# Performance work log

Measured on AMD Instinct MI355X. Metric: run time of the kernel, lower is better.

The kernel has to match this reference:

```python
import jax, jax.numpy as jnp
import numpy as np

R = 50000          # residues
P = 24             # residue_pad_length
APR = 15           # atoms per residue (<= P)
N = R * APR        # total atoms
ACD = ATD = RCD = RID = 32
N_ATOM_CODES, N_ATOM_TYPES, N_RES_CODES, MAX_SEQ = 38, 6, 21, 1024
VEC_OUT, SC_OUT = 64, 256          # irreps_out = 64x1e + 256x0e
SC_IN = P * ACD + P * ATD + RCD + RID  # 1600 scalar inputs


def setup_inputs() -> dict:
    key = jax.random.key(0)
    ks = jax.random.split(key, 10)
    return {
        "residue_base_coords": jax.random.normal(ks[0], (R, 3), jnp.float32),
        "residue_relative_coords": jax.random.normal(ks[1], (N, 3), jnp.float32),
        "residue_code_index": jax.random.randint(ks[2], (R,), 0, N_RES_CODES),
        "residue_sequence_index": jnp.arange(R) % MAX_SEQ,
        "atom_code_index": jax.random.randint(ks[3], (N,), 0, N_ATOM_CODES),
        "atom_type_index": jax.random.randint(ks[4], (N,), 0, N_ATOM_TYPES),
        "residue_index_atomwise": jnp.repeat(jnp.arange(R), APR),  # sorted, APR atoms each
        "W_atom_code": jax.random.normal(ks[5], (N_ATOM_CODES, ACD), jnp.float32),
        "W_atom_type": jax.random.normal(ks[6], (N_ATOM_TYPES, ATD), jnp.float32),
        "W_res_code": jax.random.normal(ks[7], (N_RES_CODES, RCD), jnp.float32),
        "W_res_idx": jax.random.normal(ks[8], (MAX_SEQ, RID), jnp.float32),
        "W_vec": jax.random.normal(jax.random.fold_in(key, 1), (P, VEC_OUT), jnp.float32),
        "W_sc": jax.random.normal(ks[9], (SC_IN, SC_OUT), jnp.float32),
    }


def reference(residue_base_coords, residue_relative_coords, residue_code_index,
              residue_sequence_index, atom_code_index, atom_type_index,
              residue_index_atomwise, W_atom_code, W_atom_type, W_res_code,
              W_res_idx, W_vec, W_sc):
    R_ = residue_base_coords.shape[0]
    P_ = W_vec.shape[0]
    N_ = residue_index_atomwise.shape[0]
    ri = residue_index_atomwise
    # vectorized replacement of the per-residue python loop:
    # position of each atom within its residue (residue_index_atomwise is sorted)
    offsets = jnp.searchsorted(ri, jnp.arange(R_))            # first atom of each residue
    pos = jnp.arange(N_) - offsets[ri]                        # [N]
    # scatter atoms into padded [R, P, ...] layout (pad slots stay 0, like F.pad)
    mask = jnp.zeros((R_, P_), bool).at[ri, pos].set(True)
    rel = jnp.zeros((R_, P_, 3), residue_relative_coords.dtype).at[ri, pos].set(residue_relative_coords)
    codes = jnp.zeros((R_, P_), atom_code_index.dtype).at[ri, pos].set(atom_code_index)
    types = jnp.zeros((R_, P_), atom_type_index.dtype).at[ri, pos].set(atom_type_index)
    maskf = mask.astype(W_atom_code.dtype)[..., None]
    # embedding lookups, masked (pad embeddings zeroed as in the torch code)
    ac = (W_atom_code[codes] * maskf).reshape(R_, -1)         # [R, P*ACD]
    at = (W_atom_type[types] * maskf).reshape(R_, -1)         # [R, P*ATD]
    rc = W_res_code[residue_code_index]                       # [R, RCD]
    rix = W_res_idx[residue_sequence_index]                   # [R, RID]
    scalars = jnp.concatenate([ac, at, rc, rix], axis=-1)     # [R, SC_IN]
    # e3nn o3.Linear: l=1 channels mix only with l=1 (Px1e -> VEC_OUTx1e),
    # l=0 channels mix only with l=0; path-normalized by sqrt(fan_in), no bias.
    out_vec = jnp.einsum('rpc,pm->rmc', rel, W_vec) / jnp.sqrt(jnp.float32(P_))
    out_sc = (scalars @ W_sc) / jnp.sqrt(jnp.float32(scalars.shape[-1]))
    features = jnp.concatenate([out_vec.reshape(R_, -1), out_sc], axis=-1)  # [R, 3*VEC_OUT+SC_OUT]
    return residue_base_coords, features  # ResidueState(coords, features)
```

## Files before the change

kernel.cpp:

```cpp
#include <hip/hip_runtime.h>
#include <stdint.h>

static constexpr int P       = 24;
static constexpr int EMB_D   = 32;
static constexpr int N_AC    = 38;
static constexpr int N_AT    = 6;
static constexpr int N_RC    = 21;
static constexpr int MAXSEQ  = 1024;
static constexpr int VEC_OUT = 64;
static constexpr int SC_OUT  = 256;
static constexpr int FEAT    = 3 * VEC_OUT + SC_OUT;
static constexpr int CT      = N_AC * N_AT;
static constexpr int NROWS   = P * CT;
static constexpr int ROWB    = SC_OUT * 2;
static constexpr uint32_t ZROWB = (uint32_t)NROWS * ROWB;
static constexpr uint32_t EOFS  = (uint32_t)N_RC * 512;

#define AS1 __attribute__((address_space(1)))
#define AS3 __attribute__((address_space(3)))

__device__ __forceinline__ unsigned short f2bf(float f) {
    uint32_t x = __float_as_uint(f);
    uint32_t r = (x + 0x7FFFu + ((x >> 16) & 1u)) >> 16;
    return (unsigned short)r;
}

__device__ __forceinline__ void gl_lds16(const void* g, void* l) {
    __builtin_amdgcn_global_load_lds((const AS1 void*)g, (AS3 void*)l, 16, 0, 0);
}

__global__ __launch_bounds__(256) void k1_init_build(
        const float* __restrict__ Wac, const float* __restrict__ Wat,
        const float* __restrict__ Wrc, const float* __restrict__ Wri,
        const float* __restrict__ Wsc,
        float* __restrict__ Ec, float* __restrict__ Et,
        unsigned short* __restrict__ ErcH, unsigned short* __restrict__ ErixH,
        int* __restrict__ starts, int* __restrict__ ends, int R) {
    int b = blockIdx.x;
    const int initB = (R + 255) / 256;
    if (b < initB) {
        int i = b * 256 + threadIdx.x;
        if (i < R) { starts[i] = 0; ends[i] = 0; }
        return;
    }
    b -= initB;
    const float* Wemb; int n_emb, sc_base, idx, sect;
    if (b < P * N_AC) {
        Wemb = Wac; n_emb = N_AC; sc_base = 0; idx = b; sect = 0;
    } else if (b < P * N_AC + P * N_AT) {
        Wemb = Wat; n_emb = N_AT; sc_base = P * EMB_D; idx = b - P * N_AC; sect = 1;
    } else if (b < P * N_AC + P * N_AT + N_RC) {
        Wemb = Wrc; n_emb = N_RC; sc_base = 2 * P * EMB_D;
        idx = b - (P * N_AC + P * N_AT); sect = 2;
    } else {
        Wemb = Wri; n_emb = MAXSEQ; sc_base = 2 * P * EMB_D + EMB_D;
        idx = b - (P * N_AC + P * N_AT + N_RC); sect = 3;
    }
    int p = idx / n_emb, e = idx % n_emb;
    int o = threadIdx.x;
    const float* wrow = Wemb + (size_t)e * EMB_D;
    const float* scol = Wsc + (size_t)(sc_base + p * EMB_D) * SC_OUT + o;
    float s = 0.f;
#pragma unroll
    for (int d = 0; d < EMB_D; ++d) s += wrow[d] * scol[(size_t)d * SC_OUT];
    s *= 0.025f;
    if (sect == 0)      Ec[(size_t)idx * SC_OUT + o] = s;
    else if (sect == 1) Et[(size_t)idx * SC_OUT + o] = s;
    else if (sect == 2) ErcH[(size_t)idx * SC_OUT + o] = f2bf(s);
    else                ErixH[(size_t)idx * SC_OUT + o] = f2bf(s);
}

__global__ void k2_find_bounds(const int* __restrict__ ri, int* __restrict__ starts,
                               int* __restrict__ ends, int N) {
    int i = blockIdx.x * blockDim.x + threadIdx.x;
    if (i >= N) return;
    int r = ri[i];
    if (i == 0 || ri[i - 1] != r) starts[r] = i;
    if (i == N - 1 || ri[i + 1] != r) ends[r] = i + 1;
}

__global__ __launch_bounds__(256) void k3_fuse_prep(
        const float* __restrict__ Ec, const float* __restrict__ Et,
        unsigned short* __restrict__ Etab,
        const int* __restrict__ starts, const int* __restrict__ ends,
        const int* __restrict__ rcode, const int* __restrict__ rseq,
        const int* __restrict__ acode, const int* __restrict__ atype,
        const float* __restrict__ rel, const float* __restrict__ base,
        float* __restrict__ out_coords,
        int4* __restrict__ hdr, uint32_t* __restrict__ recArr, int R) {
    int b = blockIdx.x;
    if (b < NROWS + 1) {
        int o = threadIdx.x;
        if (b == NROWS) { Etab[(size_t)b * SC_OUT + o] = 0; return; }
        int j = b / CT, ct = b % CT, c = ct / N_AT, t = ct % N_AT;
        float s = Ec[((size_t)j * N_AC + c) * SC_OUT + o] +
                  Et[((size_t)j * N_AT + t) * SC_OUT + o];
        Etab[(size_t)b * SC_OUT + o] = f2bf(s);
        return;
    }
    b -= NROWS + 1;
    const int hdrB = (R + 255) >> 8;
    if (b < hdrB) {
        int i = b * 256 + threadIdx.x;
        if (i < R) {
            int st = starts[i];
            int c = ends[i] - st; if (c > P) c = P;
            hdr[i] = make_int4(st, c, rcode[i], rseq[i]);
        }
        return;
    }
    b -= hdrB;
    const int coordB = (3 * R + 1023) >> 10;
    if (b < coordB) {
        int i = b * 256 + threadIdx.x;
        int n4 = (3 * R) >> 2;
        if (i < n4)
            reinterpret_cast<float4*>(out_coords)[i] =
                reinterpret_cast<const float4*>(base)[i];
        if (i == n4) {
            for (int t = 4 * n4; t < 3 * R; ++t) out_coords[t] = base[t];
        }
        return;
    }
    b -= coordB;
    int i = b * 256 + threadIdx.x;
    if (i >= R * 64) return;
    int r = i >> 6, l = i & 63;
    int st = starts[r];
    int c = ends[r] - st; if (c > P) c = P;
    uint32_t out;
    if (l < 16) {
        out = ZROWB;
        if (l < c)
            out = (uint32_t)((l * CT + acode[st + l] * N_AT + atype[st + l]) * ROWB);
    } else {
        int idx = l - 16, k = idx / 3, cc = idx - k * 3;
        float v = 0.f;
        if (k < c) v = rel[(size_t)(st + k) * 3 + cc];
        out = __float_as_uint(v);
    }
    recArr[(size_t)r * 64 + l] = out;
}

struct F3 { float x, y, z; };

__global__ __launch_bounds__(256, 4) void k4_residue(
        const int4* __restrict__ hdr, const uint32_t* __restrict__ recArr,
        const unsigned char* __restrict__ tab,
        const unsigned char* __restrict__ ErcBase,
        const float* __restrict__ Wvec,
        const int* __restrict__ acode, const int* __restrict__ atype,
        const float* __restrict__ rel,
        float* __restrict__ out_feat, int R) {

    __shared__ uint8_t stage[4][9 * 1024];
    const int wid    = threadIdx.x >> 6;
    const int lane   = threadIdx.x & 63;
    const int b31    = lane & 31;
    const bool hiH   = lane >= 32;
    const uint32_t lo16 = (uint32_t)(b31 * 16);
    const int wave   = (blockIdx.x << 2) + wid;
    const int totalw = gridDim.x << 2;
    if (wave >= R) return;
    uint8_t* buf = stage[wid];

    float w[16];
#pragma unroll
    for (int k = 0; k < 16; ++k) w[k] = Wvec[k * VEC_OUT + lane];

    int j = wave;
    int r0 = __builtin_amdgcn_readfirstlane(j < R ? j : R - 1);
    uint32_t rec = recArr[(size_t)r0 * 64 + lane];
    int4 h = hdr[r0];

    while (true) {
        int jn = j + totalw;
        int r1 = __builtin_amdgcn_readfirstlane(jn < R ? jn : R - 1);
        uint32_t recN = recArr[(size_t)r1 * 64 + lane];
        int4 hN = hdr[r1];

#pragma unroll
        for (int k = 0; k < 8; ++k) {
            uint32_t re = (uint32_t)__builtin_amdgcn_readlane((int)rec, 2 * k);
            uint32_t ro = (uint32_t)__builtin_amdgcn_readlane((int)rec, 2 * k + 1);
            gl_lds16(tab + (hiH ? ro : re) + lo16, buf + k * 1024);
        }
        {
            uint32_t vo = (hiH ? EOFS + ((uint32_t)h.w << 9)
                               : ((uint32_t)h.z << 9)) + lo16;
            gl_lds16(ErcBase + vo, buf + 8 * 1024);
        }

        float vx = 0.f, vy = 0.f, vz = 0.f;
#pragma unroll
        for (int k = 0; k < 16; ++k) {
            float sx = __uint_as_float((uint32_t)__builtin_amdgcn_readlane((int)rec, 16 + 3 * k));
            float sy = __uint_as_float((uint32_t)__builtin_amdgcn_readlane((int)rec, 17 + 3 * k));
            float sz = __uint_as_float((uint32_t)__builtin_amdgcn_readlane((int)rec, 18 + 3 * k));
            vx = fmaf(sx, w[k], vx);
            vy = fmaf(sy, w[k], vy);
            vz = fmaf(sz, w[k], vz);
        }

        asm volatile("s_waitcnt vmcnt(0)" ::: "memory");
        __builtin_amdgcn_sched_barrier(0);

        float a0 = 0.f, a1 = 0.f, a2 = 0.f, a3 = 0.f;
        float a4 = 0.f, a5 = 0.f, a6 = 0.f, a7 = 0.f;
#pragma unroll
        for (int k = 0; k < 9; ++k) {
            uint4 gk = *reinterpret_cast<const uint4*>(buf + k * 1024 + lane * 16);
            a0 += __uint_as_float(gk.x << 16);
            a1 += __uint_as_float(gk.x & 0xFFFF0000u);
            a2 += __uint_as_float(gk.y << 16);
            a3 += __uint_as_float(gk.y & 0xFFFF0000u);
            a4 += __uint_as_float(gk.z << 16);
            a5 += __uint_as_float(gk.z & 0xFFFF0000u);
            a6 += __uint_as_float(gk.w << 16);
            a7 += __uint_as_float(gk.w & 0xFFFF0000u);
        }

        a0 += __shfl_xor(a0, 32); a1 += __shfl_xor(a1, 32);
        a2 += __shfl_xor(a2, 32); a3 += __shfl_xor(a3, 32);
        a4 += __shfl_xor(a4, 32); a5 += __shfl_xor(a5, 32);
        a6 += __shfl_xor(a6, 32); a7 += __shfl_xor(a7, 32);

        if (h.y > 16) {
            int st = h.x;
            for (int k = 16; k < h.y; ++k) {
                int c = acode[st + k], t = atype[st + k];
                const unsigned char* rp = tab +
                    (uint32_t)((k * CT + c * N_AT + t) * ROWB) + lo16;
                uint4 gg = *reinterpret_cast<const uint4*>(rp);
                float wk = Wvec[k * VEC_OUT + lane];
                vx = fmaf(rel[(size_t)(st + k) * 3], wk, vx);
                vy = fmaf(rel[(size_t)(st + k) * 3 + 1], wk, vy);
                vz = fmaf(rel[(size_t)(st + k) * 3 + 2], wk, vz);
                float t0 = __uint_as_float(gg.x << 16);
                float t1 = __uint_as_float(gg.x & 0xFFFF0000u);
                float t2 = __uint_as_float(gg.y << 16);
                float t3 = __uint_as_float(gg.y & 0xFFFF0000u);
                float t4 = __uint_as_float(gg.z << 16);
                float t5 = __uint_as_float(gg.z & 0xFFFF0000u);
                float t6 = __uint_as_float(gg.w << 16);
                float t7 = __uint_as_float(gg.w & 0xFFFF0000u);
                a0 += t0; a1 += t1; a2 += t2; a3 += t3;
                a4 += t4; a5 += t5; a6 += t6; a7 += t7;
            }
        }

        const float vs = 0.20412414523193150818f;
        float* frow = out_feat + (size_t)j * FEAT;
        F3 v3; v3.x = vx * vs; v3.y = vy * vs; v3.z = vz * vs;
        *reinterpret_cast<F3*>(frow + 3 * lane) = v3;
        float4 sd = hiH ? make_float4(a4, a5, a6, a7)
                        : make_float4(a0, a1, a2, a3);
        uint32_t so = ((uint32_t)b31 << 5) + (hiH ? 16u : 0u);
        *reinterpret_cast<float4*>(
            reinterpret_cast<char*>(frow + 3 * VEC_OUT) + so) = sd;

        j = jn;
        if (j >= R) break;
        rec = recN; h = hN;
    }
}

extern "C" void kernel_launch(void* const* d_in, const int* in_sizes, int n_in,
                              void* d_out, int out_size, void* d_ws, size_t ws_size,
                              hipStream_t stream) {
    const float* base  = (const float*)d_in[0];
    const float* rel   = (const float*)d_in[1];
    const int*   rcode = (const int*)d_in[2];
    const int*   rseq  = (const int*)d_in[3];
    const int*   acode = (const int*)d_in[4];
    const int*   atype = (const int*)d_in[5];
    const int*   ri    = (const int*)d_in[6];
    const float* Wac   = (const float*)d_in[7];
    const float* Wat   = (const float*)d_in[8];
    const float* Wrc   = (const float*)d_in[9];
    const float* Wri   = (const float*)d_in[10];
    const float* Wv    = (const float*)d_in[11];
    const float* Wsc   = (const float*)d_in[12];

    const int R = in_sizes[0] / 3;
    const int N = in_sizes[6];

    float* out_coords = (float*)d_out;
    float* out_feat   = out_coords + (size_t)R * 3;

    char* ws = (char*)d_ws;
    size_t ofs = 0;
    auto alloc = [&](size_t bytes) {
        void* p = ws + ofs;
        ofs = (ofs + bytes + 255) & ~255ULL;
        return p;
    };
    int*            starts = (int*)alloc((size_t)R * 4);
    int*            ends   = (int*)alloc((size_t)R * 4);
    float*          Ec_f   = (float*)alloc((size_t)P * N_AC * SC_OUT * 4);
    float*          Et_f   = (float*)alloc((size_t)P * N_AT * SC_OUT * 4);
    unsigned short* ErcH   = (unsigned short*)alloc((size_t)N_RC * SC_OUT * 2);
    unsigned short* ErixH  = (unsigned short*)alloc((size_t)MAXSEQ * SC_OUT * 2);
    unsigned short* Etab   = (unsigned short*)alloc((size_t)(NROWS + 1) * SC_OUT * 2);
    int4*           hdr    = (int4*)alloc((size_t)R * 16);
    uint32_t*       recArr = (uint32_t*)alloc((size_t)R * 64 * 4);
    (void)ws_size; (void)n_in; (void)out_size;

    const int initB  = (R + 255) / 256;
    const int k1B    = initB + P * N_AC + P * N_AT + N_RC + MAXSEQ;
    const int hdrB   = (R + 255) / 256;
    const int coordB = (3 * R + 1023) / 1024;
    const int recB   = (R * 64 + 255) / 256;
    const int k3B    = (NROWS + 1) + hdrB + coordB + recB;

    k1_init_build<<<k1B, 256, 0, stream>>>(Wac, Wat, Wrc, Wri, Wsc,
                                           Ec_f, Et_f, ErcH, ErixH, starts, ends, R);
    k2_find_bounds<<<(N + 255) / 256, 256, 0, stream>>>(ri, starts, ends, N);
    k3_fuse_prep<<<k3B, 256, 0, stream>>>(Ec_f, Et_f, Etab, starts, ends,
                                          rcode, rseq, acode, atype, rel, base,
                                          out_coords, hdr, recArr, R);
    k4_residue<<<2048, 256, 0, stream>>>(
        hdr, recArr, (const unsigned char*)Etab,
        (const unsigned char*)ErcH, Wv, acode, atype, rel, out_feat, R);
}
```

Before: 60.97 us.

## Double-buffer LDS staging in residue kernel to prefetch next residue's rows

Turns the per-wave gather loop into a two-stage software pipeline. The embedding-table rows for the next residue are loaded into a second LDS buffer while the current one is reduced, and record prefetches now go through global_load_lds. Partial vmcnt waits replace the full drain. The launch also shrinks to 128-thread blocks with 1024 blocks, so there are fewer total waves and less parallelism, in exchange for hiding load latency within each wave. The hand-counted vmcnt values are fragile if the compiler emits extra memory operations such as the hdr load.

```diff
diff --git a/kernel.cpp b/kernel.cpp
--- a/kernel.cpp
+++ b/kernel.cpp
@@ -15,6 +15,8 @@
 static constexpr int ROWB    = SC_OUT * 2;
 static constexpr uint32_t ZROWB = (uint32_t)NROWS * ROWB;
 static constexpr uint32_t EOFS  = (uint32_t)N_RC * 512;
+static constexpr int BUFB  = 9 * 1024 + 256;
+static constexpr int RECOF = 9 * 1024;
 
 #define AS1 __attribute__((address_space(1)))
 #define AS3 __attribute__((address_space(3)))
@@ -27,6 +29,9 @@
 
 __device__ __forceinline__ void gl_lds16(const void* g, void* l) {
     __builtin_amdgcn_global_load_lds((const AS1 void*)g, (AS3 void*)l, 16, 0, 0);
+}
+__device__ __forceinline__ void gl_lds4(const void* g, void* l) {
+    __builtin_amdgcn_global_load_lds((const AS1 void*)g, (AS3 void*)l, 4, 0, 0);
 }
 
 __global__ __launch_bounds__(256) void k1_init_build(
@@ -144,7 +149,7 @@
 
 struct F3 { float x, y, z; };
 
-__global__ __launch_bounds__(256, 4) void k4_residue(
+__global__ __launch_bounds__(128, 2) void k4_residue(
         const int4* __restrict__ hdr, const uint32_t* __restrict__ recArr,
         const unsigned char* __restrict__ tab,
         const unsigned char* __restrict__ ErcBase,
@@ -153,63 +158,88 @@
         const float* __restrict__ rel,
         float* __restrict__ out_feat, int R) {
 
-    __shared__ uint8_t stage[4][9 * 1024];
+    __shared__ uint8_t stage[2][2][BUFB];
     const int wid    = threadIdx.x >> 6;
     const int lane   = threadIdx.x & 63;
     const int b31    = lane & 31;
     const bool hiH   = lane >= 32;
     const uint32_t lo16 = (uint32_t)(b31 * 16);
-    const int wave   = (blockIdx.x << 2) + wid;
-    const int totalw = gridDim.x << 2;
+    const int wave   = (blockIdx.x << 1) + wid;
+    const int totalw = gridDim.x << 1;
     if (wave >= R) return;
-    uint8_t* buf = stage[wid];
+    uint8_t* buf0 = stage[wid][0];
+    uint8_t* buf1 = stage[wid][1];
 
     float w[16];
 #pragma unroll
     for (int k = 0; k < 16; ++k) w[k] = Wvec[k * VEC_OUT + lane];
 
-    int j = wave;
-    int r0 = __builtin_amdgcn_readfirstlane(j < R ? j : R - 1);
-    uint32_t rec = recArr[(size_t)r0 * 64 + lane];
-    int4 h = hdr[r0];
-
+    auto ridx = [&](int jj) {
+        return __builtin_amdgcn_readfirstlane(jj < R ? jj : R - 1);
+    };
+
+    int j  = wave;
+    int r0 = ridx(j);
+    int r1 = ridx(j + totalw);
+    int4 hCur = hdr[r0];
+    int4 hNxt = hdr[r1];
+    gl_lds4(recArr + (size_t)r0 * 64 + lane, buf1 + RECOF);
+    asm volatile("s_waitcnt vmcnt(0)" ::: "memory");
+    __builtin_amdgcn_sched_barrier(0);
+    uint32_t recCur = *reinterpret_cast<const uint32_t*>(buf1 + RECOF + lane * 4);
+    gl_lds4(recArr + (size_t)r1 * 64 + lane, buf0 + RECOF);
+#pragma unroll
+    for (int k = 0; k < 8; ++k) {
+        uint32_t re = (uint32_t)__builtin_amdgcn_readlane((int)recCur, 2 * k);
+        uint32_t ro = (uint32_t)__builtin_amdgcn_readlane((int)recCur, 2 * k + 1);
+        gl_lds16(tab + (hiH ? ro : re) + lo16, buf0 + k * 1024);
+    }
+    gl_lds16(ErcBase + (hiH ? EOFS + ((uint32_t)hCur.w << 9)
+                            : ((uint32_t)hCur.z << 9)) + lo16, buf0 + 8 * 1024);
+
+    int cur = 0;
     while (true) {
+        uint8_t* bc = cur ? buf1 : buf0;
+        uint8_t* bn = cur ? buf0 : buf1;
+
+        asm volatile("s_waitcnt vmcnt(9)" ::: "memory");
+        __builtin_amdgcn_sched_barrier(0);
+
+        uint32_t recNxt = *reinterpret_cast<const uint32_t*>(bc + RECOF + lane * 4);
+
         int jn = j + totalw;
-        int r1 = __builtin_amdgcn_readfirstlane(jn < R ? jn : R - 1);
-        uint32_t recN = recArr[(size_t)r1 * 64 + lane];
-        int4 hN = hdr[r1];
+        int r2 = ridx(j + 2 * totalw);
+        gl_lds4(recArr + (size_t)r2 * 64 + lane, bn + RECOF);
+        int4 h2 = hdr[r2];
 
 #pragma unroll
         for (int k = 0; k < 8; ++k) {
-            uint32_t re = (uint32_t)__builtin_amdgcn_readlane((int)rec, 2 * k);
-            uint32_t ro = (uint32_t)__builtin_amdgcn_readlane((int)rec, 2 * k + 1);
-            gl_lds16(tab + (hiH ? ro : re) + lo16, buf + k * 1024);
-        }
-        {
-            uint32_t vo = (hiH ? EOFS + ((uint32_t)h.w << 9)
-                               : ((uint32_t)h.z << 9)) + lo16;
-            gl_lds16(ErcBase + vo, buf + 8 * 1024);
-        }
+            uint32_t re = (uint32_t)__builtin_amdgcn_readlane((int)recNxt, 2 * k);
+            uint32_t ro = (uint32_t)__builtin_amdgcn_readlane((int)recNxt, 2 * k + 1);
+            gl_lds16(tab + (hiH ? ro : re) + lo16, bn + k * 1024);
+        }
+        gl_lds16(ErcBase + (hiH ? EOFS + ((uint32_t)hNxt.w << 9)
+                                : ((uint32_t)hNxt.z << 9)) + lo16, bn + 8 * 1024);
 
         float vx = 0.f, vy = 0.f, vz = 0.f;
 #pragma unroll
         for (int k = 0; k < 16; ++k) {
-            float sx = __uint_as_float((uint32_t)__builtin_amdgcn_readlane((int)rec, 16 + 3 * k));
-            float sy = __uint_as_float((uint32_t)__builtin_amdgcn_readlane((int)rec, 17 + 3 * k));
-            float sz = __uint_as_float((uint32_t)__builtin_amdgcn_readlane((int)rec, 18 + 3 * k));
+            float sx = __uint_as_float((uint32_t)__builtin_amdgcn_readlane((int)recCur, 16 + 3 * k));
+            float sy = __uint_as_float((uint32_t)__builtin_amdgcn_readlane((int)recCur, 17 + 3 * k));
+            float sz = __uint_as_float((uint32_t)__builtin_amdgcn_readlane((int)recCur, 18 + 3 * k));
             vx = fmaf(sx, w[k], vx);
             vy = fmaf(sy, w[k], vy);
             vz = fmaf(sz, w[k], vz);
         }
 
-        asm volatile("s_waitcnt vmcnt(0)" ::: "memory");
+        asm volatile("s_waitcnt vmcnt(10)" ::: "memory");
         __builtin_amdgcn_sched_barrier(0);
 
         float a0 = 0.f, a1 = 0.f, a2 = 0.f, a3 = 0.f;
         float a4 = 0.f, a5 = 0.f, a6 = 0.f, a7 = 0.f;
 #pragma unroll
         for (int k = 0; k < 9; ++k) {
-            uint4 gk = *reinterpret_cast<const uint4*>(buf + k * 1024 + lane * 16);
+            uint4 gk = *reinterpret_cast<const uint4*>(bc + k * 1024 + lane * 16);
             a0 += __uint_as_float(gk.x << 16);
             a1 += __uint_as_float(gk.x & 0xFFFF0000u);
             a2 += __uint_as_float(gk.y << 16);
@@ -219,15 +249,14 @@
             a6 += __uint_as_float(gk.w << 16);
             a7 += __uint_as_float(gk.w & 0xFFFF0000u);
         }
-
         a0 += __shfl_xor(a0, 32); a1 += __shfl_xor(a1, 32);
         a2 += __shfl_xor(a2, 32); a3 += __shfl_xor(a3, 32);
         a4 += __shfl_xor(a4, 32); a5 += __shfl_xor(a5, 32);
         a6 += __shfl_xor(a6, 32); a7 += __shfl_xor(a7, 32);
 
-        if (h.y > 16) {
-            int st = h.x;
-            for (int k = 16; k < h.y; ++k) {
+        if (hCur.y > 16) {
+            int st = hCur.x;
+            for (int k = 16; k < hCur.y; ++k) {
                 int c = acode[st + k], t = atype[st + k];
                 const unsigned char* rp = tab +
                     (uint32_t)((k * CT + c * N_AT + t) * ROWB) + lo16;
@@ -236,16 +265,14 @@
                 vx = fmaf(rel[(size_t)(st + k) * 3], wk, vx);
                 vy = fmaf(rel[(size_t)(st + k) * 3 + 1], wk, vy);
                 vz = fmaf(rel[(size_t)(st + k) * 3 + 2], wk, vz);
-                float t0 = __uint_as_float(gg.x << 16);
-                float t1 = __uint_as_float(gg.x & 0xFFFF0000u);
-                float t2 = __uint_as_float(gg.y << 16);
-                float t3 = __uint_as_float(gg.y & 0xFFFF0000u);
-                float t4 = __uint_as_float(gg.z << 16);
-                float t5 = __uint_as_float(gg.z & 0xFFFF0000u);
-                float t6 = __uint_as_float(gg.w << 16);
-                float t7 = __uint_as_float(gg.w & 0xFFFF0000u);
-                a0 += t0; a1 += t1; a2 += t2; a3 += t3;
-                a4 += t4; a5 += t5; a6 += t6; a7 += t7;
+                a0 += __uint_as_float(gg.x << 16);
+                a1 += __uint_as_float(gg.x & 0xFFFF0000u);
+                a2 += __uint_as_float(gg.y << 16);
+                a3 += __uint_as_float(gg.y & 0xFFFF0000u);
+                a4 += __uint_as_float(gg.z << 16);
+                a5 += __uint_as_float(gg.z & 0xFFFF0000u);
+                a6 += __uint_as_float(gg.w << 16);
+                a7 += __uint_as_float(gg.w & 0xFFFF0000u);
             }
         }
 
@@ -261,7 +288,7 @@
 
         j = jn;
         if (j >= R) break;
-        rec = recN; h = hN;
+        recCur = recNxt; hCur = hNxt; hNxt = h2; cur ^= 1;
     }
 }
 
@@ -319,7 +346,7 @@
     k3_fuse_prep<<<k3B, 256, 0, stream>>>(Ec_f, Et_f, Etab, starts, ends,
                                           rcode, rseq, acode, atype, rel, base,
                                           out_coords, hdr, recArr, R);
-    k4_residue<<<2048, 256, 0, stream>>>(
+    k4_residue<<<1024, 128, 0, stream>>>(
         hdr, recArr, (const unsigned char*)Etab,
         (const unsigned char*)ErcH, Wv, acode, atype, rel, out_feat, R);
 }
```

New measurement: 67.47 us. 10.7% more time.
